# Optimization experiments

Hardware: AMD Instinct MI355X
Metric: run time of the kernel (lower is better)

Reference implementation:

```python
import jax, jax.numpy as jnp
import numpy as np

B, S, H, NH = 4, 4096, 1024, 16
HD = H // NH  # head_dim = 64


def setup_inputs() -> dict:
    key = jax.random.key(0)
    ks = jax.random.split(key, 8)
    scale = 0.02
    return {
        "hidden_states": jax.random.normal(ks[0], (B, S, H), dtype=jnp.float32),
        "attention_mask": jnp.ones((B, S), dtype=jnp.float32),
        "Wq": jax.random.normal(ks[1], (H, H), dtype=jnp.float32) * scale,
        "bq": jnp.zeros((H,), dtype=jnp.float32),
        "Wk": jax.random.normal(ks[2], (H, H), dtype=jnp.float32) * scale,
        "bk": jnp.zeros((H,), dtype=jnp.float32),
        "Wv": jax.random.normal(ks[3], (H, H), dtype=jnp.float32) * scale,
        "bv": jnp.zeros((H,), dtype=jnp.float32),
        "Wo": jax.random.normal(ks[4], (H, H), dtype=jnp.float32) * scale,
        "bo": jnp.zeros((H,), dtype=jnp.float32),
    }


def _heads(x):
    # [B,S,H] -> [B,NH,S,HD]
    b, s, _ = x.shape
    return x.reshape(b, s, NH, HD).transpose(0, 2, 1, 3)


def reference(hidden_states, attention_mask, Wq, bq, Wk, bk, Wv, bv, Wo, bo):
    b, s, _ = hidden_states.shape
    q = _heads(hidden_states @ Wq.T + bq)
    k = _heads(hidden_states @ Wk.T + bk)
    v = _heads(hidden_states @ Wv.T + bv)

    m = attention_mask[:, None, :, None]  # [B,1,S,1]
    k = k * m
    v = v * m

    # Faithful to the torch code: kv_i = matmul(k_i[b,h,1,d], v_i[b,h,d,1])
    # is the SCALAR dot product k_t . v_t, broadcast-added to the [d,d] state.
    # => state_t = (cumsum_t k_t.v_t) * ones(d,d)
    # => o_t = state_t @ q_t = (cumsum_t k_t.v_t) * sum_j q_t[j], same for every i.
    dots = jnp.einsum('bhsd,bhsd->bhs', k, v)        # scalar k.v per step
    cum = jnp.cumsum(dots, axis=-1)                  # running state scalar
    qsum = jnp.sum(q, axis=-1)                       # [B,NH,S]
    o = jnp.broadcast_to((cum * qsum)[..., None], q.shape)  # [B,NH,S,HD]

    out = o.transpose(0, 2, 1, 3).reshape(b, s, NH * HD)
    out = out @ Wo.T + bo  # dropout is identity (eval / p handled as 0)

    # final state: last cumulative scalar broadcast over the [d,d] matrix
    state = jnp.broadcast_to(cum[:, :, -1, None, None], (b, NH, HD, HD))
    return out, state
```

## Files before the change

kernel.cpp:

```cpp
#include <hip/hip_runtime.h>


typedef __attribute__((ext_vector_type(4))) float f32x4;
typedef __attribute__((ext_vector_type(8))) short bf16x8;
typedef __attribute__((ext_vector_type(8))) unsigned short u16x8;
typedef unsigned int u32;

#define GLDS16(g, l)                                                            \
  __builtin_amdgcn_global_load_lds((const __attribute__((address_space(1))) u32*)(g), \
                                   (__attribute__((address_space(3))) u32*)(l), 16, 0, 0)
#define MFMA16(a, b, c) __builtin_amdgcn_mfma_f32_16x16x32_bf16(a, b, c, 0, 0, 0)
#define PH_BAR __builtin_amdgcn_s_barrier()
#define LGK0 do { asm volatile("s_waitcnt lgkmcnt(0)" ::: "memory"); \
                  __builtin_amdgcn_sched_barrier(0); } while (0)

__device__ __forceinline__ unsigned short f2bf(float f) {
  union { float f; u32 u; } x; x.f = f;
  u32 r = (x.u + 0x7fffu + ((x.u >> 16) & 1u)) >> 16;
  return (unsigned short)r;
}

__global__ void k_prep(const float* __restrict__ X, unsigned short* __restrict__ Xb,
                       const float* __restrict__ Wq, const float* __restrict__ bq,
                       const float* __restrict__ Wk, const float* __restrict__ bk,
                       const float* __restrict__ Wv, const float* __restrict__ bv,
                       const float* __restrict__ Wo,
                       unsigned short* __restrict__ Wkb, unsigned short* __restrict__ Wvb,
                       unsigned short* __restrict__ SWb, float* __restrict__ WosT,
                       float* __restrict__ scal) {
  int blk = blockIdx.x, t = threadIdx.x;
  if (blk < 2048) {
    const float* src = (blk < 1024) ? Wk : Wv;
    unsigned short* dst = (blk < 1024) ? Wkb : Wvb;
    size_t i = ((size_t)(blk & 1023) * 256 + t) * 4;
    f32x4 v = *(const f32x4*)(src + i);
    dst[i + 0] = f2bf(v.x); dst[i + 1] = f2bf(v.y);
    dst[i + 2] = f2bf(v.z); dst[i + 3] = f2bf(v.w);
  } else if (blk < 2241) {
    int b2 = blk - 2048;
    if (b2 < 128) {
      int o = b2 * 256 + t;
      int r = o >> 10, c = o & 1023;
      float s = 0.f;
      if (r < 16) {
        for (int d = 0; d < 64; ++d) s += Wq[(size_t)(r * 64 + d) * 1024 + c];
      } else {
        int h = r - 16;
        for (int d = 0; d < 64; ++d) {
          int j = h * 64 + d;
          s += bv[j] * Wk[(size_t)j * 1024 + c] + bk[j] * Wv[(size_t)j * 1024 + c];
        }
      }
      SWb[o] = f2bf(s);
    } else if (b2 < 192) {
      int o = (b2 - 128) * 256 + t;
      int h = o >> 10, j = o & 1023;
      float s = 0.f;
      for (int d = 0; d < 64; ++d) s += Wo[(size_t)j * 1024 + h * 64 + d];
      WosT[o] = s;
    } else {
      if (t < 16) {
        float s = 0.f;
        for (int d = 0; d < 64; ++d) s += bq[t * 64 + d];
        scal[t] = s;
      } else if (t < 32) {
        int h = t - 16;
        float s = 0.f;
        for (int d = 0; d < 64; ++d) s += bk[h * 64 + d] * bv[h * 64 + d];
        scal[t] = s;
      }
    }
  } else {
    size_t i = ((size_t)(blk - 2241) * 256 + t) * 8;
    f32x4 a = *(const f32x4*)(X + i);
    f32x4 b = *(const f32x4*)(X + i + 4);
    u16x8 o;
    o[0] = f2bf(a.x); o[1] = f2bf(a.y); o[2] = f2bf(a.z); o[3] = f2bf(a.w);
    o[4] = f2bf(b.x); o[5] = f2bf(b.y); o[6] = f2bf(b.z); o[7] = f2bf(b.w);
    *(u16x8*)(Xb + i) = o;
  }
}

#define NT 32
#define BUFS 17408
__global__ __launch_bounds__(512, 1) void k_dualgemm(
    const unsigned short* __restrict__ Xb,
    const unsigned short* __restrict__ Wkb,
    const unsigned short* __restrict__ Wvb,
    const unsigned short* __restrict__ SWb,
    float* __restrict__ dotsT, float* __restrict__ qsumT, float* __restrict__ dotbT) {
  extern __shared__ __align__(16) unsigned short lds[];
  int orig = blockIdx.x;
  int wg = (orig & 7) * 64 + (orig >> 3);
  int bx = wg & 7, by = wg >> 3;
  int row0 = by << 8, col0 = bx << 7;
  int tid = threadIdx.x, wid = tid >> 6, lane = tid & 63;
  int wrM = wid >> 1, wcN = wid & 1;
  int fr = lane & 15, fg = lane >> 4;
  bool side = (bx == 0);

  int uA0 = tid, uA1 = tid + 512;
  const unsigned short* sA0 = Xb + (size_t)(row0 + (uA0 >> 2)) * 1024 + (((uA0 & 3) ^ ((uA0 >> 3) & 3)) << 3);
  const unsigned short* sA1 = Xb + (size_t)(row0 + (uA1 >> 2)) * 1024 + (((uA1 & 3) ^ ((uA1 >> 3) & 3)) << 3);
  const unsigned short* sK  = Wkb + (size_t)(col0 + (tid >> 2)) * 1024 + (((tid & 3) ^ ((tid >> 3) & 3)) << 3);
  const unsigned short* sV  = Wvb + (size_t)(col0 + (tid >> 2)) * 1024 + (((tid & 3) ^ ((tid >> 3) & 3)) << 3);
  const unsigned short* sS  = SWb + (size_t)(tid >> 2) * 1024 + (((tid & 3) ^ ((tid >> 3) & 3)) << 3);
  int dA0 = wid << 9, dA1 = 4096 + (wid << 9);
  int dK = 8192 + (wid << 9), dV = 12288 + (wid << 9);
  int dS = 16384 + (wid << 9);
  bool stageSW = side && (wid < 2);

  int xsw = (fg ^ ((fr >> 1) & 3)) << 3;
  int aro = (wrM * 64 + fr) * 32 + xsw;
  int bro = (wcN * 64 + fr) * 32 + xsw;
  int swo = 16384 + (wcN * 16 + fr) * 32 + xsw;

  f32x4 ck[4][4] = {{0}}, cv[4][4] = {{0}};
  f32x4 qa[4] = {0, 0, 0, 0};

#pragma unroll
  for (int p = 0; p < 3; ++p) {
    int bb = p * BUFS, ko = p * 32;
    GLDS16(sA0 + ko, lds + bb + dA0);
    GLDS16(sK + ko, lds + bb + dK);
    GLDS16(sA1 + ko, lds + bb + dA1);
    GLDS16(sV + ko, lds + bb + dV);
    if (stageSW) GLDS16(sS + ko, lds + bb + dS);
  }
  asm volatile("s_waitcnt vmcnt(8)" ::: "memory");
  PH_BAR;

  for (int t = 0; t < NT; ++t) {
    const int rb = (t & 3) * BUFS;
    const int t3 = t + 3;
    const int bb = (t3 & 3) * BUFS;
    const int ko = t3 << 5;
    const bool st = (t3 < NT);
    bf16x8 a[4], bk[4], bv[4];

#pragma unroll
    for (int mi = 0; mi < 4; ++mi) a[mi] = *(const bf16x8*)(lds + rb + aro + mi * 512);
#pragma unroll
    for (int ni = 0; ni < 4; ++ni) bk[ni] = *(const bf16x8*)(lds + rb + 8192 + bro + ni * 512);
    if (st) {
      GLDS16(sA0 + ko, lds + bb + dA0);
      GLDS16(sK + ko, lds + bb + dK);
    }
    PH_BAR; LGK0;
    __builtin_amdgcn_s_setprio(1);
#pragma unroll
    for (int mi = 0; mi < 4; ++mi)
#pragma unroll
      for (int ni = 0; ni < 4; ++ni)
        ck[mi][ni] = MFMA16(a[mi], bk[ni], ck[mi][ni]);
    __builtin_amdgcn_s_setprio(0);
    PH_BAR;

#pragma unroll
    for (int ni = 0; ni < 4; ++ni) bv[ni] = *(const bf16x8*)(lds + rb + 12288 + bro + ni * 512);
    bf16x8 sw;
    if (side) sw = *(const bf16x8*)(lds + rb + swo);
    if (st) {
      GLDS16(sA1 + ko, lds + bb + dA1);
      GLDS16(sV + ko, lds + bb + dV);
      if (stageSW) GLDS16(sS + ko, lds + bb + dS);
    }
    PH_BAR; LGK0;
    __builtin_amdgcn_s_setprio(1);
#pragma unroll
    for (int mi = 0; mi < 4; ++mi)
#pragma unroll
      for (int ni = 0; ni < 4; ++ni)
        cv[mi][ni] = MFMA16(a[mi], bv[ni], cv[mi][ni]);
    if (side) {
#pragma unroll
      for (int mi = 0; mi < 4; ++mi) qa[mi] = MFMA16(a[mi], sw, qa[mi]);
    }
    __builtin_amdgcn_s_setprio(0);
    if (t <= NT - 4)      { asm volatile("s_waitcnt vmcnt(8)" ::: "memory"); }
    else if (t == NT - 3) { asm volatile("s_waitcnt vmcnt(4)" ::: "memory"); }
    else                  { asm volatile("s_waitcnt vmcnt(0)" ::: "memory"); }
    PH_BAR;
  }

  float part[4][4];
#pragma unroll
  for (int mi = 0; mi < 4; ++mi)
#pragma unroll
    for (int q = 0; q < 4; ++q) {
      float s = 0.f;
#pragma unroll
      for (int ni = 0; ni < 4; ++ni) s += ck[mi][ni][q] * cv[mi][ni][q];
      part[mi][q] = s;
    }
#pragma unroll
  for (int r = 0; r < 4; ++r) {
#pragma unroll
    for (int mi = 0; mi < 4; ++mi)
#pragma unroll
      for (int q = 0; q < 4; ++q)
        part[mi][q] += __shfl_xor(part[mi][q], 1 << r, 64);
  }
  int h = bx * 2 + wcN;
  if (fr == 0) {
#pragma unroll
    for (int mi = 0; mi < 4; ++mi)
#pragma unroll
      for (int q = 0; q < 4; ++q)
        dotsT[(size_t)h * 16384 + row0 + wrM * 64 + mi * 16 + fg * 4 + q] = part[mi][q];
  }
  if (side) {
    float* dst = (wcN == 0) ? qsumT : dotbT;
#pragma unroll
    for (int mi = 0; mi < 4; ++mi)
#pragma unroll
      for (int q = 0; q < 4; ++q)
        dst[(size_t)fr * 16384 + row0 + wrM * 64 + mi * 16 + fg * 4 + q] = qa[mi][q];
  }
}

__global__ void k_cumsum(const float* __restrict__ dotsT, const float* __restrict__ dotbT,
                         const float* __restrict__ qsumT, const float* __restrict__ scal,
                         const float* __restrict__ mask,
                         float* __restrict__ coef, float* __restrict__ state) {
  __shared__ float csum[256];
  int b = blockIdx.x >> 4, h = blockIdx.x & 15;
  int t = threadIdx.x;
  float bqs = scal[h], dbc = scal[16 + h];
  size_t m0 = (size_t)b * 4096;
  const float* dro = dotsT + (size_t)h * 16384 + m0;
  const float* dbo = dotbT + (size_t)h * 16384 + m0;
  const float* qso = qsumT + (size_t)h * 16384 + m0;
  const float* mko = mask + m0;
  float loc[16], run = 0.f;
  int s0 = t * 16;
#pragma unroll
  for (int i = 0; i < 16; ++i) {
    int ii = s0 + i;
    float mk = mko[ii];
    float d = (dro[ii] + dbo[ii] + dbc) * mk * mk;
    run += d;
    loc[i] = run;
  }
  csum[t] = run;
  __syncthreads();
  for (int off = 1; off < 256; off <<= 1) {
    float v = (t >= off) ? csum[t - off] : 0.f;
    __syncthreads();
    csum[t] += v;
    __syncthreads();
  }
  float prefix = csum[t] - run;
#pragma unroll
  for (int i = 0; i < 16; ++i) {
    int ii = s0 + i;
    float cum = prefix + loc[i];
    coef[(m0 + ii) * 16 + h] = cum * (qso[ii] + bqs);
  }
  float total = csum[255];
  float* sp = state + (size_t)(b * 16 + h) * 4096;
  for (int i = t; i < 4096; i += 256) sp[i] = total;
}

__global__ __launch_bounds__(256) void k_outgemm(const float* __restrict__ coef,
                                                 const float* __restrict__ WosT,
                                                 const float* __restrict__ bo,
                                                 float* __restrict__ out) {
  int t = threadIdx.x;
  int j0 = t * 4;
  f32x4 w4[16];
#pragma unroll
  for (int hh = 0; hh < 16; ++hh) w4[hh] = *(const f32x4*)&WosT[hh * 1024 + j0];
  f32x4 bov = *(const f32x4*)&bo[j0];
  size_t m0 = (size_t)blockIdx.x * 32;
  for (int mi = 0; mi < 32; ++mi) {
    size_t m = m0 + mi;
    const float* cm = &coef[m * 16];
    f32x4 acc = bov;
#pragma unroll
    for (int hh = 0; hh < 16; ++hh) acc += w4[hh] * cm[hh];
    *(f32x4*)&out[m * 1024 + j0] = acc;
  }
}

extern "C" void kernel_launch(void* const* d_in, const int* in_sizes, int n_in,
                              void* d_out, int out_size, void* d_ws, size_t ws_size,
                              hipStream_t stream) {
  const float* X    = (const float*)d_in[0];
  const float* mask = (const float*)d_in[1];
  const float* Wq   = (const float*)d_in[2];
  const float* bq   = (const float*)d_in[3];
  const float* Wk   = (const float*)d_in[4];
  const float* bk   = (const float*)d_in[5];
  const float* Wv   = (const float*)d_in[6];
  const float* bv   = (const float*)d_in[7];
  const float* Wo   = (const float*)d_in[8];
  const float* bo   = (const float*)d_in[9];
  float* out   = (float*)d_out;
  float* state = out + (size_t)16384 * 1024;

  char* w = (char*)d_ws;
  unsigned short* Xb  = (unsigned short*)w; w += (size_t)16384 * 1024 * 2;
  unsigned short* Wkb = (unsigned short*)w; w += (size_t)1024 * 1024 * 2;
  unsigned short* Wvb = (unsigned short*)w; w += (size_t)1024 * 1024 * 2;
  unsigned short* SWb = (unsigned short*)w; w += (size_t)32 * 1024 * 2;
  float* WosT  = (float*)w; w += (size_t)16 * 1024 * 4;
  float* scal  = (float*)w; w += 256;
  float* dotsT = (float*)w; w += (size_t)16 * 16384 * 4;
  float* qsumT = (float*)w; w += (size_t)16 * 16384 * 4;
  float* dotbT = (float*)w; w += (size_t)16 * 16384 * 4;
  float* coef  = (float*)w; w += (size_t)16384 * 16 * 4;

  (void)hipFuncSetAttribute((const void*)k_dualgemm,
                            hipFuncAttributeMaxDynamicSharedMemorySize, 139264);

  hipLaunchKernelGGL(k_prep,     dim3(10433), dim3(256), 0, stream,
                     X, Xb, Wq, bq, Wk, bk, Wv, bv, Wo, Wkb, Wvb, SWb, WosT, scal);
  hipLaunchKernelGGL(k_dualgemm, dim3(512),  dim3(512), 139264, stream, Xb, Wkb, Wvb, SWb,
                     dotsT, qsumT, dotbT);
  hipLaunchKernelGGL(k_cumsum,   dim3(64),   dim3(256), 0, stream, dotsT, dotbT, qsumT, scal,
                     mask, coef, state);
  hipLaunchKernelGGL(k_outgemm,  dim3(512),  dim3(256), 0, stream, coef, WosT, bo, out);
}
```

Measured before the change: 116.1 us.

## Switch dual GEMM to BK=64 double-buffered pipeline with one barrier per step

The K-loop of the fused K/V projection GEMM now takes 64-wide K tiles over 16 steps instead of 32-wide tiles over 32 steps. The 4-stage ring with split A0/A1 phases is replaced by a 2-stage double buffer. The next tile is issued at the top of each step and waited for with vmcnt(0) plus one barrier at the end, and the K and V MFMAs are interleaved within each half-tile using an 8-way XOR swizzle. This is meant to cut barrier count and phase serialization per K element. In exchange, prefetch depth drops to one stage, which may expose global latency, and the LDS footprint per stage doubles.

```diff
diff --git a/kernel.cpp b/kernel.cpp
--- a/kernel.cpp
+++ b/kernel.cpp
@@ -81,8 +81,8 @@
   }
 }
 
-#define NT 32
-#define BUFS 17408
+#define NT 16
+#define BUFS 34816
 __global__ __launch_bounds__(512, 1) void k_dualgemm(
     const unsigned short* __restrict__ Xb,
     const unsigned short* __restrict__ Wkb,
@@ -98,88 +98,113 @@
   int wrM = wid >> 1, wcN = wid & 1;
   int fr = lane & 15, fg = lane >> 4;
   bool side = (bx == 0);
-
-  int uA0 = tid, uA1 = tid + 512;
-  const unsigned short* sA0 = Xb + (size_t)(row0 + (uA0 >> 2)) * 1024 + (((uA0 & 3) ^ ((uA0 >> 3) & 3)) << 3);
-  const unsigned short* sA1 = Xb + (size_t)(row0 + (uA1 >> 2)) * 1024 + (((uA1 & 3) ^ ((uA1 >> 3) & 3)) << 3);
-  const unsigned short* sK  = Wkb + (size_t)(col0 + (tid >> 2)) * 1024 + (((tid & 3) ^ ((tid >> 3) & 3)) << 3);
-  const unsigned short* sV  = Wvb + (size_t)(col0 + (tid >> 2)) * 1024 + (((tid & 3) ^ ((tid >> 3) & 3)) << 3);
-  const unsigned short* sS  = SWb + (size_t)(tid >> 2) * 1024 + (((tid & 3) ^ ((tid >> 3) & 3)) << 3);
-  int dA0 = wid << 9, dA1 = 4096 + (wid << 9);
-  int dK = 8192 + (wid << 9), dV = 12288 + (wid << 9);
-  int dS = 16384 + (wid << 9);
-  bool stageSW = side && (wid < 2);
-
-  int xsw = (fg ^ ((fr >> 1) & 3)) << 3;
-  int aro = (wrM * 64 + fr) * 32 + xsw;
-  int bro = (wcN * 64 + fr) * 32 + xsw;
-  int swo = 16384 + (wcN * 16 + fr) * 32 + xsw;
+  bool stageSW = side && (wid < 4);
+  int dW = wid << 9;
+
+  const unsigned short *sA[4], *sK[2], *sV[2], *sS;
+#pragma unroll
+  for (int c = 0; c < 4; ++c) {
+    int U = c * 512 + tid, r = U >> 3;
+    sA[c] = Xb + (size_t)(row0 + r) * 1024 + (((U & 7) ^ (r & 7)) << 3);
+  }
+#pragma unroll
+  for (int c = 0; c < 2; ++c) {
+    int U = c * 512 + tid, r = U >> 3;
+    int usw = ((U & 7) ^ (r & 7)) << 3;
+    sK[c] = Wkb + (size_t)(col0 + r) * 1024 + usw;
+    sV[c] = Wvb + (size_t)(col0 + r) * 1024 + usw;
+  }
+  {
+    int U = tid & 255, r = U >> 3;
+    sS = SWb + (size_t)r * 1024 + (((U & 7) ^ (r & 7)) << 3);
+  }
+
+  int arow = wrM * 64 + fr;
+  int brow = wcN * 64 + fr;
+  int srow = wcN * 16 + fr;
+  int f7 = fr & 7;
+  int u0 = ((0 * 4 + fg) ^ f7) << 3;
+  int u1 = ((1 * 4 + fg) ^ f7) << 3;
 
   f32x4 ck[4][4] = {{0}}, cv[4][4] = {{0}};
   f32x4 qa[4] = {0, 0, 0, 0};
 
-#pragma unroll
-  for (int p = 0; p < 3; ++p) {
-    int bb = p * BUFS, ko = p * 32;
-    GLDS16(sA0 + ko, lds + bb + dA0);
-    GLDS16(sK + ko, lds + bb + dK);
-    GLDS16(sA1 + ko, lds + bb + dA1);
-    GLDS16(sV + ko, lds + bb + dV);
-    if (stageSW) GLDS16(sS + ko, lds + bb + dS);
-  }
-  asm volatile("s_waitcnt vmcnt(8)" ::: "memory");
-  PH_BAR;
+  {
+#pragma unroll
+    for (int c = 0; c < 4; ++c) GLDS16(sA[c], lds + c * 4096 + dW);
+#pragma unroll
+    for (int c = 0; c < 2; ++c) {
+      GLDS16(sK[c], lds + 16384 + c * 4096 + dW);
+      GLDS16(sV[c], lds + 24576 + c * 4096 + dW);
+    }
+    if (stageSW) GLDS16(sS, lds + 32768 + dW);
+    asm volatile("s_waitcnt vmcnt(0)" ::: "memory");
+    PH_BAR;
+  }
 
   for (int t = 0; t < NT; ++t) {
-    const int rb = (t & 3) * BUFS;
-    const int t3 = t + 3;
-    const int bb = (t3 & 3) * BUFS;
-    const int ko = t3 << 5;
-    const bool st = (t3 < NT);
-    bf16x8 a[4], bk[4], bv[4];
-
-#pragma unroll
-    for (int mi = 0; mi < 4; ++mi) a[mi] = *(const bf16x8*)(lds + rb + aro + mi * 512);
-#pragma unroll
-    for (int ni = 0; ni < 4; ++ni) bk[ni] = *(const bf16x8*)(lds + rb + 8192 + bro + ni * 512);
-    if (st) {
-      GLDS16(sA0 + ko, lds + bb + dA0);
-      GLDS16(sK + ko, lds + bb + dK);
-    }
-    PH_BAR; LGK0;
+    const int rb = (t & 1) * BUFS;
+    const int wb = ((t + 1) & 1) * BUFS;
+    const int ko = (t + 1) << 6;
+    if (t + 1 < NT) {
+#pragma unroll
+      for (int c = 0; c < 4; ++c) GLDS16(sA[c] + ko, lds + wb + c * 4096 + dW);
+#pragma unroll
+      for (int c = 0; c < 2; ++c) {
+        GLDS16(sK[c] + ko, lds + wb + 16384 + c * 4096 + dW);
+        GLDS16(sV[c] + ko, lds + wb + 24576 + c * 4096 + dW);
+      }
+      if (stageSW) GLDS16(sS + ko, lds + wb + 32768 + dW);
+    }
+
+    bf16x8 a[4], bk[4], bv[4], sw;
+#pragma unroll
+    for (int mi = 0; mi < 4; ++mi) a[mi] = *(const bf16x8*)(lds + rb + (arow + mi * 16) * 64 + u0);
+#pragma unroll
+    for (int ni = 0; ni < 4; ++ni) {
+      bk[ni] = *(const bf16x8*)(lds + rb + 16384 + (brow + ni * 16) * 64 + u0);
+      bv[ni] = *(const bf16x8*)(lds + rb + 24576 + (brow + ni * 16) * 64 + u0);
+    }
+    if (side) sw = *(const bf16x8*)(lds + rb + 32768 + srow * 64 + u0);
+    LGK0;
     __builtin_amdgcn_s_setprio(1);
 #pragma unroll
     for (int mi = 0; mi < 4; ++mi)
 #pragma unroll
-      for (int ni = 0; ni < 4; ++ni)
+      for (int ni = 0; ni < 4; ++ni) {
         ck[mi][ni] = MFMA16(a[mi], bk[ni], ck[mi][ni]);
+        cv[mi][ni] = MFMA16(a[mi], bv[ni], cv[mi][ni]);
+      }
+    if (side) {
+#pragma unroll
+      for (int mi = 0; mi < 4; ++mi) qa[mi] = MFMA16(a[mi], sw, qa[mi]);
+    }
     __builtin_amdgcn_s_setprio(0);
-    PH_BAR;
-
-#pragma unroll
-    for (int ni = 0; ni < 4; ++ni) bv[ni] = *(const bf16x8*)(lds + rb + 12288 + bro + ni * 512);
-    bf16x8 sw;
-    if (side) sw = *(const bf16x8*)(lds + rb + swo);
-    if (st) {
-      GLDS16(sA1 + ko, lds + bb + dA1);
-      GLDS16(sV + ko, lds + bb + dV);
-      if (stageSW) GLDS16(sS + ko, lds + bb + dS);
-    }
-    PH_BAR; LGK0;
+
+#pragma unroll
+    for (int mi = 0; mi < 4; ++mi) a[mi] = *(const bf16x8*)(lds + rb + (arow + mi * 16) * 64 + u1);
+#pragma unroll
+    for (int ni = 0; ni < 4; ++ni) {
+      bk[ni] = *(const bf16x8*)(lds + rb + 16384 + (brow + ni * 16) * 64 + u1);
+      bv[ni] = *(const bf16x8*)(lds + rb + 24576 + (brow + ni * 16) * 64 + u1);
+    }
+    if (side) sw = *(const bf16x8*)(lds + rb + 32768 + srow * 64 + u1);
+    LGK0;
     __builtin_amdgcn_s_setprio(1);
 #pragma unroll
     for (int mi = 0; mi < 4; ++mi)
 #pragma unroll
-      for (int ni = 0; ni < 4; ++ni)
+      for (int ni = 0; ni < 4; ++ni) {
+        ck[mi][ni] = MFMA16(a[mi], bk[ni], ck[mi][ni]);
         cv[mi][ni] = MFMA16(a[mi], bv[ni], cv[mi][ni]);
+      }
     if (side) {
 #pragma unroll
       for (int mi = 0; mi < 4; ++mi) qa[mi] = MFMA16(a[mi], sw, qa[mi]);
     }
     __builtin_amdgcn_s_setprio(0);
-    if (t <= NT - 4)      { asm volatile("s_waitcnt vmcnt(8)" ::: "memory"); }
-    else if (t == NT - 3) { asm volatile("s_waitcnt vmcnt(4)" ::: "memory"); }
-    else                  { asm volatile("s_waitcnt vmcnt(0)" ::: "memory"); }
+
+    asm volatile("s_waitcnt vmcnt(0)" ::: "memory");
     PH_BAR;
   }
 
```

Result: faster. 108.0 us (-7.0%).

## Shrink dual-GEMM tiles, split side GEMM into separate blocks, double-buffer

Applied to the files above, without the earlier changes.

The K/V dual GEMM moves from 256x128 tiles with a 4-stage buffer and one block per CU to 256x64 tiles with a 2-stage buffer. Shared memory per block drops to 48 KB and launch bounds now allow 4 blocks per CU. The q-sum and bias-dot side GEMM, which used to run inside the bx==0 blocks and unbalanced them, gets its own 64 blocks. Each head's dot now comes as two partial sums that the cumsum kernel adds together. In exchange, the deeper prefetch pipeline is lost, a full vmcnt(0) wait sits in every iteration, and X is read from global memory twice as often.

```diff
diff --git a/kernel.cpp b/kernel.cpp
--- a/kernel.cpp
+++ b/kernel.cpp
@@ -10,9 +10,6 @@
   __builtin_amdgcn_global_load_lds((const __attribute__((address_space(1))) u32*)(g), \
                                    (__attribute__((address_space(3))) u32*)(l), 16, 0, 0)
 #define MFMA16(a, b, c) __builtin_amdgcn_mfma_f32_16x16x32_bf16(a, b, c, 0, 0, 0)
-#define PH_BAR __builtin_amdgcn_s_barrier()
-#define LGK0 do { asm volatile("s_waitcnt lgkmcnt(0)" ::: "memory"); \
-                  __builtin_amdgcn_sched_barrier(0); } while (0)
 
 __device__ __forceinline__ unsigned short f2bf(float f) {
   union { float f; u32 u; } x; x.f = f;
@@ -82,105 +79,131 @@
 }
 
 #define NT 32
-#define BUFS 17408
-__global__ __launch_bounds__(512, 1) void k_dualgemm(
+#define BUFS 12288
+__global__ __launch_bounds__(512, 4) void k_dualgemm(
     const unsigned short* __restrict__ Xb,
     const unsigned short* __restrict__ Wkb,
     const unsigned short* __restrict__ Wvb,
     const unsigned short* __restrict__ SWb,
-    float* __restrict__ dotsT, float* __restrict__ qsumT, float* __restrict__ dotbT) {
+    float* __restrict__ dots2, float* __restrict__ qsumT, float* __restrict__ dotbT) {
   extern __shared__ __align__(16) unsigned short lds[];
   int orig = blockIdx.x;
-  int wg = (orig & 7) * 64 + (orig >> 3);
-  int bx = wg & 7, by = wg >> 3;
-  int row0 = by << 8, col0 = bx << 7;
   int tid = threadIdx.x, wid = tid >> 6, lane = tid & 63;
+  int fr = lane & 15, fg = lane >> 4;
+  int u_r = (fg ^ (fr & 3)) << 3;
+
+  if (orig >= 1024) {
+    int rowblk = orig - 1024;
+    int row0 = rowblk << 8;
+    int U0 = tid, r0 = U0 >> 2;
+    int U1 = tid + 512, r1 = U1 >> 2;
+    const unsigned short* sA0 = Xb + (size_t)(row0 + r0) * 1024 + (((U0 & 3) ^ (r0 & 3)) << 3);
+    const unsigned short* sA1 = Xb + (size_t)(row0 + r1) * 1024 + (((U1 & 3) ^ (r1 & 3)) << 3);
+    int Us0 = lane, rs0 = Us0 >> 2;
+    int Us1 = 64 + lane, rs1 = Us1 >> 2;
+    const unsigned short* sS0 = SWb + (size_t)rs0 * 1024 + (((Us0 & 3) ^ (rs0 & 3)) << 3);
+    const unsigned short* sS1 = SWb + (size_t)rs1 * 1024 + (((Us1 & 3) ^ (rs1 & 3)) << 3);
+    int dA0 = wid << 9, dA1 = 4096 + (wid << 9);
+    f32x4 acc[2][2] = {{0}};
+    int aoff0 = (wid * 32 + fr) * 32 + u_r;
+    int aoff1 = (wid * 32 + 16 + fr) * 32 + u_r;
+    int soff0 = 8192 + fr * 32 + u_r;
+    int soff1 = 8192 + (16 + fr) * 32 + u_r;
+    GLDS16(sA0, lds + dA0);
+    GLDS16(sA1, lds + dA1);
+    if (wid == 0) { GLDS16(sS0, lds + 8192); GLDS16(sS1, lds + 8192 + 512); }
+    asm volatile("s_waitcnt vmcnt(0)" ::: "memory");
+    __builtin_amdgcn_s_barrier();
+    for (int t = 0; t < NT; ++t) {
+      int rb = (t & 1) * BUFS, wb = ((t + 1) & 1) * BUFS, ko = (t + 1) << 5;
+      if (t + 1 < NT) {
+        GLDS16(sA0 + ko, lds + wb + dA0);
+        GLDS16(sA1 + ko, lds + wb + dA1);
+        if (wid == 0) { GLDS16(sS0 + ko, lds + wb + 8192); GLDS16(sS1 + ko, lds + wb + 8192 + 512); }
+      }
+      bf16x8 a0 = *(const bf16x8*)(lds + rb + aoff0);
+      bf16x8 a1 = *(const bf16x8*)(lds + rb + aoff1);
+      bf16x8 s0 = *(const bf16x8*)(lds + rb + soff0);
+      bf16x8 s1 = *(const bf16x8*)(lds + rb + soff1);
+      acc[0][0] = MFMA16(a0, s0, acc[0][0]);
+      acc[0][1] = MFMA16(a0, s1, acc[0][1]);
+      acc[1][0] = MFMA16(a1, s0, acc[1][0]);
+      acc[1][1] = MFMA16(a1, s1, acc[1][1]);
+      asm volatile("s_waitcnt vmcnt(0)" ::: "memory");
+      __builtin_amdgcn_s_barrier();
+    }
+    size_t mbase = row0 + wid * 32;
+#pragma unroll
+    for (int mi = 0; mi < 2; ++mi)
+#pragma unroll
+      for (int ni = 0; ni < 2; ++ni) {
+        float* dst = (ni == 0) ? qsumT : dotbT;
+#pragma unroll
+        for (int q = 0; q < 4; ++q)
+          dst[(size_t)fr * 16384 + mbase + mi * 16 + fg * 4 + q] = acc[mi][ni][q];
+      }
+    return;
+  }
+
+  int wg = (orig & 7) * 128 + (orig >> 3);
+  int bx = wg & 15, by = wg >> 4;
+  int row0 = by << 8, col0 = bx << 6;
   int wrM = wid >> 1, wcN = wid & 1;
-  int fr = lane & 15, fg = lane >> 4;
-  bool side = (bx == 0);
-
-  int uA0 = tid, uA1 = tid + 512;
-  const unsigned short* sA0 = Xb + (size_t)(row0 + (uA0 >> 2)) * 1024 + (((uA0 & 3) ^ ((uA0 >> 3) & 3)) << 3);
-  const unsigned short* sA1 = Xb + (size_t)(row0 + (uA1 >> 2)) * 1024 + (((uA1 & 3) ^ ((uA1 >> 3) & 3)) << 3);
-  const unsigned short* sK  = Wkb + (size_t)(col0 + (tid >> 2)) * 1024 + (((tid & 3) ^ ((tid >> 3) & 3)) << 3);
-  const unsigned short* sV  = Wvb + (size_t)(col0 + (tid >> 2)) * 1024 + (((tid & 3) ^ ((tid >> 3) & 3)) << 3);
-  const unsigned short* sS  = SWb + (size_t)(tid >> 2) * 1024 + (((tid & 3) ^ ((tid >> 3) & 3)) << 3);
+
+  int U0 = tid, r0 = U0 >> 2;
+  int U1 = tid + 512, r1 = U1 >> 2;
+  const unsigned short* sA0 = Xb + (size_t)(row0 + r0) * 1024 + (((U0 & 3) ^ (r0 & 3)) << 3);
+  const unsigned short* sA1 = Xb + (size_t)(row0 + r1) * 1024 + (((U1 & 3) ^ (r1 & 3)) << 3);
+  int Ub = tid & 255, rB = Ub >> 2;
+  int uswB = ((Ub & 3) ^ (rB & 3)) << 3;
+  const unsigned short* sB = (wid < 4) ? (Wkb + (size_t)(col0 + rB) * 1024 + uswB)
+                                       : (Wvb + (size_t)(col0 + rB) * 1024 + uswB);
   int dA0 = wid << 9, dA1 = 4096 + (wid << 9);
-  int dK = 8192 + (wid << 9), dV = 12288 + (wid << 9);
-  int dS = 16384 + (wid << 9);
-  bool stageSW = side && (wid < 2);
-
-  int xsw = (fg ^ ((fr >> 1) & 3)) << 3;
-  int aro = (wrM * 64 + fr) * 32 + xsw;
-  int bro = (wcN * 64 + fr) * 32 + xsw;
-  int swo = 16384 + (wcN * 16 + fr) * 32 + xsw;
-
-  f32x4 ck[4][4] = {{0}}, cv[4][4] = {{0}};
-  f32x4 qa[4] = {0, 0, 0, 0};
-
-#pragma unroll
-  for (int p = 0; p < 3; ++p) {
-    int bb = p * BUFS, ko = p * 32;
-    GLDS16(sA0 + ko, lds + bb + dA0);
-    GLDS16(sK + ko, lds + bb + dK);
-    GLDS16(sA1 + ko, lds + bb + dA1);
-    GLDS16(sV + ko, lds + bb + dV);
-    if (stageSW) GLDS16(sS + ko, lds + bb + dS);
-  }
-  asm volatile("s_waitcnt vmcnt(8)" ::: "memory");
-  PH_BAR;
+  int dB = ((wid < 4) ? 8192 : 10240) + ((wid & 3) << 9);
+
+  int aoff[4], bkoff[2], bvoff[2];
+#pragma unroll
+  for (int mi = 0; mi < 4; ++mi) aoff[mi] = (wrM * 64 + mi * 16 + fr) * 32 + u_r;
+#pragma unroll
+  for (int ni = 0; ni < 2; ++ni) {
+    bkoff[ni] = 8192 + (wcN * 32 + ni * 16 + fr) * 32 + u_r;
+    bvoff[ni] = 10240 + (wcN * 32 + ni * 16 + fr) * 32 + u_r;
+  }
+
+  f32x4 ck[4][2] = {{0}}, cv[4][2] = {{0}};
+
+  GLDS16(sA0, lds + dA0);
+  GLDS16(sA1, lds + dA1);
+  GLDS16(sB, lds + dB);
+  asm volatile("s_waitcnt vmcnt(0)" ::: "memory");
+  __builtin_amdgcn_s_barrier();
 
   for (int t = 0; t < NT; ++t) {
-    const int rb = (t & 3) * BUFS;
-    const int t3 = t + 3;
-    const int bb = (t3 & 3) * BUFS;
-    const int ko = t3 << 5;
-    const bool st = (t3 < NT);
-    bf16x8 a[4], bk[4], bv[4];
-
-#pragma unroll
-    for (int mi = 0; mi < 4; ++mi) a[mi] = *(const bf16x8*)(lds + rb + aro + mi * 512);
-#pragma unroll
-    for (int ni = 0; ni < 4; ++ni) bk[ni] = *(const bf16x8*)(lds + rb + 8192 + bro + ni * 512);
-    if (st) {
-      GLDS16(sA0 + ko, lds + bb + dA0);
-      GLDS16(sK + ko, lds + bb + dK);
-    }
-    PH_BAR; LGK0;
+    int rb = (t & 1) * BUFS, wb = ((t + 1) & 1) * BUFS, ko = (t + 1) << 5;
+    if (t + 1 < NT) {
+      GLDS16(sA0 + ko, lds + wb + dA0);
+      GLDS16(sA1 + ko, lds + wb + dA1);
+      GLDS16(sB + ko, lds + wb + dB);
+    }
+    bf16x8 a[4], bk[2], bv[2];
+#pragma unroll
+    for (int mi = 0; mi < 4; ++mi) a[mi] = *(const bf16x8*)(lds + rb + aoff[mi]);
+#pragma unroll
+    for (int ni = 0; ni < 2; ++ni) {
+      bk[ni] = *(const bf16x8*)(lds + rb + bkoff[ni]);
+      bv[ni] = *(const bf16x8*)(lds + rb + bvoff[ni]);
+    }
     __builtin_amdgcn_s_setprio(1);
 #pragma unroll
     for (int mi = 0; mi < 4; ++mi)
 #pragma unroll
-      for (int ni = 0; ni < 4; ++ni)
+      for (int ni = 0; ni < 2; ++ni) {
         ck[mi][ni] = MFMA16(a[mi], bk[ni], ck[mi][ni]);
+        cv[mi][ni] = MFMA16(a[mi], bv[ni], cv[mi][ni]);
+      }
     __builtin_amdgcn_s_setprio(0);
-    PH_BAR;
-
-#pragma unroll
-    for (int ni = 0; ni < 4; ++ni) bv[ni] = *(const bf16x8*)(lds + rb + 12288 + bro + ni * 512);
-    bf16x8 sw;
-    if (side) sw = *(const bf16x8*)(lds + rb + swo);
-    if (st) {
-      GLDS16(sA1 + ko, lds + bb + dA1);
-      GLDS16(sV + ko, lds + bb + dV);
-      if (stageSW) GLDS16(sS + ko, lds + bb + dS);
-    }
-    PH_BAR; LGK0;
-    __builtin_amdgcn_s_setprio(1);
-#pragma unroll
-    for (int mi = 0; mi < 4; ++mi)
-#pragma unroll
-      for (int ni = 0; ni < 4; ++ni)
-        cv[mi][ni] = MFMA16(a[mi], bv[ni], cv[mi][ni]);
-    if (side) {
-#pragma unroll
-      for (int mi = 0; mi < 4; ++mi) qa[mi] = MFMA16(a[mi], sw, qa[mi]);
-    }
-    __builtin_amdgcn_s_setprio(0);
-    if (t <= NT - 4)      { asm volatile("s_waitcnt vmcnt(8)" ::: "memory"); }
-    else if (t == NT - 3) { asm volatile("s_waitcnt vmcnt(4)" ::: "memory"); }
-    else                  { asm volatile("s_waitcnt vmcnt(0)" ::: "memory"); }
-    PH_BAR;
+    asm volatile("s_waitcnt vmcnt(0)" ::: "memory");
+    __builtin_amdgcn_s_barrier();
   }
 
   float part[4][4];
@@ -190,7 +213,7 @@
     for (int q = 0; q < 4; ++q) {
       float s = 0.f;
 #pragma unroll
-      for (int ni = 0; ni < 4; ++ni) s += ck[mi][ni][q] * cv[mi][ni][q];
+      for (int ni = 0; ni < 2; ++ni) s += ck[mi][ni][q] * cv[mi][ni][q];
       part[mi][q] = s;
     }
 #pragma unroll
@@ -201,25 +224,17 @@
       for (int q = 0; q < 4; ++q)
         part[mi][q] += __shfl_xor(part[mi][q], 1 << r, 64);
   }
-  int h = bx * 2 + wcN;
   if (fr == 0) {
 #pragma unroll
     for (int mi = 0; mi < 4; ++mi)
 #pragma unroll
       for (int q = 0; q < 4; ++q)
-        dotsT[(size_t)h * 16384 + row0 + wrM * 64 + mi * 16 + fg * 4 + q] = part[mi][q];
-  }
-  if (side) {
-    float* dst = (wcN == 0) ? qsumT : dotbT;
-#pragma unroll
-    for (int mi = 0; mi < 4; ++mi)
-#pragma unroll
-      for (int q = 0; q < 4; ++q)
-        dst[(size_t)fr * 16384 + row0 + wrM * 64 + mi * 16 + fg * 4 + q] = qa[mi][q];
-  }
-}
-
-__global__ void k_cumsum(const float* __restrict__ dotsT, const float* __restrict__ dotbT,
+        dots2[(size_t)(bx * 2 + wcN) * 16384 + row0 + wrM * 64 + mi * 16 + fg * 4 + q] =
+            part[mi][q];
+  }
+}
+
+__global__ void k_cumsum(const float* __restrict__ dots2, const float* __restrict__ dotbT,
                          const float* __restrict__ qsumT, const float* __restrict__ scal,
                          const float* __restrict__ mask,
                          float* __restrict__ coef, float* __restrict__ state) {
@@ -228,7 +243,8 @@
   int t = threadIdx.x;
   float bqs = scal[h], dbc = scal[16 + h];
   size_t m0 = (size_t)b * 4096;
-  const float* dro = dotsT + (size_t)h * 16384 + m0;
+  const float* d0 = dots2 + (size_t)(h * 2) * 16384 + m0;
+  const float* d1 = dots2 + (size_t)(h * 2 + 1) * 16384 + m0;
   const float* dbo = dotbT + (size_t)h * 16384 + m0;
   const float* qso = qsumT + (size_t)h * 16384 + m0;
   const float* mko = mask + m0;
@@ -238,7 +254,7 @@
   for (int i = 0; i < 16; ++i) {
     int ii = s0 + i;
     float mk = mko[ii];
-    float d = (dro[ii] + dbo[ii] + dbc) * mk * mk;
+    float d = (d0[ii] + d1[ii] + dbo[ii] + dbc) * mk * mk;
     run += d;
     loc[i] = run;
   }
@@ -306,19 +322,19 @@
   unsigned short* SWb = (unsigned short*)w; w += (size_t)32 * 1024 * 2;
   float* WosT  = (float*)w; w += (size_t)16 * 1024 * 4;
   float* scal  = (float*)w; w += 256;
-  float* dotsT = (float*)w; w += (size_t)16 * 16384 * 4;
+  float* dots2 = (float*)w; w += (size_t)32 * 16384 * 4;
   float* qsumT = (float*)w; w += (size_t)16 * 16384 * 4;
   float* dotbT = (float*)w; w += (size_t)16 * 16384 * 4;
   float* coef  = (float*)w; w += (size_t)16384 * 16 * 4;
 
   (void)hipFuncSetAttribute((const void*)k_dualgemm,
-                            hipFuncAttributeMaxDynamicSharedMemorySize, 139264);
+                            hipFuncAttributeMaxDynamicSharedMemorySize, 49152);
 
   hipLaunchKernelGGL(k_prep,     dim3(10433), dim3(256), 0, stream,
                      X, Xb, Wq, bq, Wk, bk, Wv, bv, Wo, Wkb, Wvb, SWb, WosT, scal);
-  hipLaunchKernelGGL(k_dualgemm, dim3(512),  dim3(512), 139264, stream, Xb, Wkb, Wvb, SWb,
-                     dotsT, qsumT, dotbT);
-  hipLaunchKernelGGL(k_cumsum,   dim3(64),   dim3(256), 0, stream, dotsT, dotbT, qsumT, scal,
+  hipLaunchKernelGGL(k_dualgemm, dim3(1088), dim3(512), 49152, stream, Xb, Wkb, Wvb, SWb,
+                     dots2, qsumT, dotbT);
+  hipLaunchKernelGGL(k_cumsum,   dim3(64),   dim3(256), 0, stream, dots2, dotbT, qsumT, scal,
                      mask, coef, state);
   hipLaunchKernelGGL(k_outgemm,  dim3(512),  dim3(256), 0, stream, coef, WosT, bo, out);
 }
```

Measured after the change: 126.7 us. 1.09x slower.

## Fuse fp32-to-bf16 conversion of X into the dual GEMM load path

Applied to the files above, without the earlier changes.

Removes the separate pass that converted the 64 MB fp32 hidden states to a bf16 workspace copy. The dual GEMM now streams fp32 X straight into LDS and packs it to bf16 in registers before the MFMAs. The pipeline also changes from a 4-buffer, 3-deep prefetch to a 3-buffer, 2-deep ring with fewer barriers per k-step. The trade-off is that each A tile now moves twice the bytes through global memory and LDS, and 150 KB of LDS is requested per block. That amount leaves room for only one block per CU regardless of the launch-bounds hint.

```diff
diff --git a/kernel.cpp b/kernel.cpp
--- a/kernel.cpp
+++ b/kernel.cpp
@@ -1,4 +1,5 @@
 #include <hip/hip_runtime.h>
+#include <hip/hip_bf16.h>
 
 
 typedef __attribute__((ext_vector_type(4))) float f32x4;
@@ -10,7 +11,6 @@
   __builtin_amdgcn_global_load_lds((const __attribute__((address_space(1))) u32*)(g), \
                                    (__attribute__((address_space(3))) u32*)(l), 16, 0, 0)
 #define MFMA16(a, b, c) __builtin_amdgcn_mfma_f32_16x16x32_bf16(a, b, c, 0, 0, 0)
-#define PH_BAR __builtin_amdgcn_s_barrier()
 #define LGK0 do { asm volatile("s_waitcnt lgkmcnt(0)" ::: "memory"); \
                   __builtin_amdgcn_sched_barrier(0); } while (0)
 
@@ -20,8 +20,17 @@
   return (unsigned short)r;
 }
 
-__global__ void k_prep(const float* __restrict__ X, unsigned short* __restrict__ Xb,
-                       const float* __restrict__ Wq, const float* __restrict__ bq,
+__device__ __forceinline__ bf16x8 pack8(const f32x4& lo, const f32x4& hi) {
+  union { bf16x8 v; u32 w[4]; } r;
+  union { __hip_bfloat162 h; u32 u; } c;
+  c.h = __float22bfloat162_rn(make_float2(lo.x, lo.y)); r.w[0] = c.u;
+  c.h = __float22bfloat162_rn(make_float2(lo.z, lo.w)); r.w[1] = c.u;
+  c.h = __float22bfloat162_rn(make_float2(hi.x, hi.y)); r.w[2] = c.u;
+  c.h = __float22bfloat162_rn(make_float2(hi.z, hi.w)); r.w[3] = c.u;
+  return r.v;
+}
+
+__global__ void k_prep(const float* __restrict__ Wq, const float* __restrict__ bq,
                        const float* __restrict__ Wk, const float* __restrict__ bk,
                        const float* __restrict__ Wv, const float* __restrict__ bv,
                        const float* __restrict__ Wo,
@@ -36,7 +45,7 @@
     f32x4 v = *(const f32x4*)(src + i);
     dst[i + 0] = f2bf(v.x); dst[i + 1] = f2bf(v.y);
     dst[i + 2] = f2bf(v.z); dst[i + 3] = f2bf(v.w);
-  } else if (blk < 2241) {
+  } else {
     int b2 = blk - 2048;
     if (b2 < 128) {
       int o = b2 * 256 + t;
@@ -70,26 +79,20 @@
         scal[t] = s;
       }
     }
-  } else {
-    size_t i = ((size_t)(blk - 2241) * 256 + t) * 8;
-    f32x4 a = *(const f32x4*)(X + i);
-    f32x4 b = *(const f32x4*)(X + i + 4);
-    u16x8 o;
-    o[0] = f2bf(a.x); o[1] = f2bf(a.y); o[2] = f2bf(a.z); o[3] = f2bf(a.w);
-    o[4] = f2bf(b.x); o[5] = f2bf(b.y); o[6] = f2bf(b.z); o[7] = f2bf(b.w);
-    *(u16x8*)(Xb + i) = o;
   }
 }
 
 #define NT 32
-#define BUFS 17408
-__global__ __launch_bounds__(512, 1) void k_dualgemm(
-    const unsigned short* __restrict__ Xb,
+__global__ __launch_bounds__(512, 2) void k_dualgemm(
+    const float* __restrict__ X,
     const unsigned short* __restrict__ Wkb,
     const unsigned short* __restrict__ Wvb,
     const unsigned short* __restrict__ SWb,
     float* __restrict__ dotsT, float* __restrict__ qsumT, float* __restrict__ dotbT) {
-  extern __shared__ __align__(16) unsigned short lds[];
+  extern __shared__ __align__(16) char ldsb[];
+  float* Af = (float*)ldsb;
+  unsigned short* Bb = (unsigned short*)(ldsb + 98304);
+  unsigned short* Sw = (unsigned short*)(ldsb + 147456);
   int orig = blockIdx.x;
   int wg = (orig & 7) * 64 + (orig >> 3);
   int bx = wg & 7, by = wg >> 3;
@@ -98,55 +101,84 @@
   int wrM = wid >> 1, wcN = wid & 1;
   int fr = lane & 15, fg = lane >> 4;
   bool side = (bx == 0);
-
-  int uA0 = tid, uA1 = tid + 512;
-  const unsigned short* sA0 = Xb + (size_t)(row0 + (uA0 >> 2)) * 1024 + (((uA0 & 3) ^ ((uA0 >> 3) & 3)) << 3);
-  const unsigned short* sA1 = Xb + (size_t)(row0 + (uA1 >> 2)) * 1024 + (((uA1 & 3) ^ ((uA1 >> 3) & 3)) << 3);
-  const unsigned short* sK  = Wkb + (size_t)(col0 + (tid >> 2)) * 1024 + (((tid & 3) ^ ((tid >> 3) & 3)) << 3);
-  const unsigned short* sV  = Wvb + (size_t)(col0 + (tid >> 2)) * 1024 + (((tid & 3) ^ ((tid >> 3) & 3)) << 3);
-  const unsigned short* sS  = SWb + (size_t)(tid >> 2) * 1024 + (((tid & 3) ^ ((tid >> 3) & 3)) << 3);
-  int dA0 = wid << 9, dA1 = 4096 + (wid << 9);
-  int dK = 8192 + (wid << 9), dV = 12288 + (wid << 9);
-  int dS = 16384 + (wid << 9);
   bool stageSW = side && (wid < 2);
 
-  int xsw = (fg ^ ((fr >> 1) & 3)) << 3;
-  int aro = (wrM * 64 + fr) * 32 + xsw;
-  int bro = (wcN * 64 + fr) * 32 + xsw;
-  int swo = 16384 + (wcN * 16 + fr) * 32 + xsw;
+  const float* sA[4];
+#pragma unroll
+  for (int c = 0; c < 4; ++c) {
+    int U = c * 512 + tid, r = U >> 3, g = (U & 7) ^ (r & 7);
+    sA[c] = X + (size_t)(row0 + r) * 1024 + g * 4;
+  }
+  const unsigned short *sK, *sV, *sS;
+  {
+    int r = tid >> 2, s = tid & 3, g = s ^ ((r >> 1) & 3);
+    sK = Wkb + (size_t)(col0 + r) * 1024 + g * 8;
+    sV = Wvb + (size_t)(col0 + r) * 1024 + g * 8;
+    int rs = (tid & 127) >> 2, ss = tid & 3, gs = ss ^ ((rs >> 1) & 3);
+    sS = SWb + (size_t)rs * 1024 + gs * 8;
+  }
+  int dA = tid << 2;
+  int dB = tid << 3;
+  int dS = tid << 3;
+
+  int keyA = fr & 7, s0 = (2 * fg) ^ keyA;
+  int aoffL[4], aoffH[4];
+#pragma unroll
+  for (int mi = 0; mi < 4; ++mi) {
+    int R = wrM * 64 + mi * 16 + fr;
+    aoffL[mi] = R * 32 + s0 * 4;
+    aoffH[mi] = R * 32 + (s0 ^ 1) * 4;
+  }
+  int ubo = (fg ^ ((fr >> 1) & 3)) << 3;
+  int bko[4], bvo[4];
+#pragma unroll
+  for (int ni = 0; ni < 4; ++ni) {
+    bko[ni] = (wcN * 64 + ni * 16 + fr) * 32 + ubo;
+    bvo[ni] = 4096 + (wcN * 64 + ni * 16 + fr) * 32 + ubo;
+  }
+  int swo = (wcN * 16 + fr) * 32 + ubo;
 
   f32x4 ck[4][4] = {{0}}, cv[4][4] = {{0}};
   f32x4 qa[4] = {0, 0, 0, 0};
 
 #pragma unroll
-  for (int p = 0; p < 3; ++p) {
-    int bb = p * BUFS, ko = p * 32;
-    GLDS16(sA0 + ko, lds + bb + dA0);
-    GLDS16(sK + ko, lds + bb + dK);
-    GLDS16(sA1 + ko, lds + bb + dA1);
-    GLDS16(sV + ko, lds + bb + dV);
-    if (stageSW) GLDS16(sS + ko, lds + bb + dS);
-  }
-  asm volatile("s_waitcnt vmcnt(8)" ::: "memory");
-  PH_BAR;
-
+  for (int p = 0; p < 2; ++p) {
+    int ko = p << 5;
+#pragma unroll
+    for (int c = 0; c < 4; ++c) GLDS16(sA[c] + ko, Af + p * 8192 + c * 2048 + dA);
+    GLDS16(sK + ko, Bb + p * 8192 + dB);
+    GLDS16(sV + ko, Bb + p * 8192 + 4096 + dB);
+    if (stageSW) GLDS16(sS + ko, Sw + p * 1024 + dS);
+  }
+  asm volatile("s_waitcnt vmcnt(6)" ::: "memory");
+  __builtin_amdgcn_s_barrier();
+
+  int bufR = 0;
   for (int t = 0; t < NT; ++t) {
-    const int rb = (t & 3) * BUFS;
-    const int t3 = t + 3;
-    const int bb = (t3 & 3) * BUFS;
-    const int ko = t3 << 5;
-    const bool st = (t3 < NT);
-    bf16x8 a[4], bk[4], bv[4];
-
-#pragma unroll
-    for (int mi = 0; mi < 4; ++mi) a[mi] = *(const bf16x8*)(lds + rb + aro + mi * 512);
-#pragma unroll
-    for (int ni = 0; ni < 4; ++ni) bk[ni] = *(const bf16x8*)(lds + rb + 8192 + bro + ni * 512);
+    const float* ArB = Af + bufR * 8192;
+    const unsigned short* BkB = Bb + bufR * 8192;
+    const unsigned short* SwB = Sw + bufR * 1024;
+    const int bufW = (bufR + 2 >= 3) ? bufR - 1 : bufR + 2;
+    const int ko = (t + 2) << 5;
+    const bool st = (t + 2 < NT);
+
+    f32x4 alo[4], ahi[4];
+#pragma unroll
+    for (int mi = 0; mi < 4; ++mi) {
+      alo[mi] = *(const f32x4*)(ArB + aoffL[mi]);
+      ahi[mi] = *(const f32x4*)(ArB + aoffH[mi]);
+    }
     if (st) {
-      GLDS16(sA0 + ko, lds + bb + dA0);
-      GLDS16(sK + ko, lds + bb + dK);
-    }
-    PH_BAR; LGK0;
+#pragma unroll
+      for (int c = 0; c < 4; ++c) GLDS16(sA[c] + ko, Af + bufW * 8192 + c * 2048 + dA);
+    }
+    bf16x8 bk[4];
+#pragma unroll
+    for (int ni = 0; ni < 4; ++ni) bk[ni] = *(const bf16x8*)(BkB + bko[ni]);
+    LGK0;
+    bf16x8 a[4];
+#pragma unroll
+    for (int mi = 0; mi < 4; ++mi) a[mi] = pack8(alo[mi], ahi[mi]);
     __builtin_amdgcn_s_setprio(1);
 #pragma unroll
     for (int mi = 0; mi < 4; ++mi)
@@ -154,18 +186,17 @@
       for (int ni = 0; ni < 4; ++ni)
         ck[mi][ni] = MFMA16(a[mi], bk[ni], ck[mi][ni]);
     __builtin_amdgcn_s_setprio(0);
-    PH_BAR;
-
-#pragma unroll
-    for (int ni = 0; ni < 4; ++ni) bv[ni] = *(const bf16x8*)(lds + rb + 12288 + bro + ni * 512);
-    bf16x8 sw;
-    if (side) sw = *(const bf16x8*)(lds + rb + swo);
+
+    bf16x8 bv[4], sw;
+#pragma unroll
+    for (int ni = 0; ni < 4; ++ni) bv[ni] = *(const bf16x8*)(BkB + bvo[ni]);
+    if (side) sw = *(const bf16x8*)(SwB + swo);
     if (st) {
-      GLDS16(sA1 + ko, lds + bb + dA1);
-      GLDS16(sV + ko, lds + bb + dV);
-      if (stageSW) GLDS16(sS + ko, lds + bb + dS);
-    }
-    PH_BAR; LGK0;
+      GLDS16(sK + ko, Bb + bufW * 8192 + dB);
+      GLDS16(sV + ko, Bb + bufW * 8192 + 4096 + dB);
+      if (stageSW) GLDS16(sS + ko, Sw + bufW * 1024 + dS);
+    }
+    LGK0;
     __builtin_amdgcn_s_setprio(1);
 #pragma unroll
     for (int mi = 0; mi < 4; ++mi)
@@ -177,10 +208,11 @@
       for (int mi = 0; mi < 4; ++mi) qa[mi] = MFMA16(a[mi], sw, qa[mi]);
     }
     __builtin_amdgcn_s_setprio(0);
-    if (t <= NT - 4)      { asm volatile("s_waitcnt vmcnt(8)" ::: "memory"); }
-    else if (t == NT - 3) { asm volatile("s_waitcnt vmcnt(4)" ::: "memory"); }
-    else                  { asm volatile("s_waitcnt vmcnt(0)" ::: "memory"); }
-    PH_BAR;
+
+    if (t <= NT - 3) { asm volatile("s_waitcnt vmcnt(6)" ::: "memory"); }
+    else             { asm volatile("s_waitcnt vmcnt(0)" ::: "memory"); }
+    __builtin_amdgcn_s_barrier();
+    bufR = (bufR + 1 >= 3) ? 0 : bufR + 1;
   }
 
   float part[4][4];
@@ -300,7 +332,6 @@
   float* state = out + (size_t)16384 * 1024;
 
   char* w = (char*)d_ws;
-  unsigned short* Xb  = (unsigned short*)w; w += (size_t)16384 * 1024 * 2;
   unsigned short* Wkb = (unsigned short*)w; w += (size_t)1024 * 1024 * 2;
   unsigned short* Wvb = (unsigned short*)w; w += (size_t)1024 * 1024 * 2;
   unsigned short* SWb = (unsigned short*)w; w += (size_t)32 * 1024 * 2;
@@ -312,11 +343,11 @@
   float* coef  = (float*)w; w += (size_t)16384 * 16 * 4;
 
   (void)hipFuncSetAttribute((const void*)k_dualgemm,
-                            hipFuncAttributeMaxDynamicSharedMemorySize, 139264);
-
-  hipLaunchKernelGGL(k_prep,     dim3(10433), dim3(256), 0, stream,
-                     X, Xb, Wq, bq, Wk, bk, Wv, bv, Wo, Wkb, Wvb, SWb, WosT, scal);
-  hipLaunchKernelGGL(k_dualgemm, dim3(512),  dim3(512), 139264, stream, Xb, Wkb, Wvb, SWb,
+                            hipFuncAttributeMaxDynamicSharedMemorySize, 153600);
+
+  hipLaunchKernelGGL(k_prep,     dim3(2241), dim3(256), 0, stream,
+                     Wq, bq, Wk, bk, Wv, bv, Wo, Wkb, Wvb, SWb, WosT, scal);
+  hipLaunchKernelGGL(k_dualgemm, dim3(512),  dim3(512), 153600, stream, X, Wkb, Wvb, SWb,
                      dotsT, qsumT, dotbT);
   hipLaunchKernelGGL(k_cumsum,   dim3(64),   dim3(256), 0, stream, dotsT, dotbT, qsumT, scal,
                      mask, coef, state);
```

After: 118.3 us. Within noise of the previous version (+1.9%).
